# Kernel tuning notes

Hardware: AMD Instinct MI355X
Metric: run time of the kernel (lower is better)

Reference implementation:

```python
import jax, jax.numpy as jnp
import numpy as np

N = 50000        # nodes
E_RAND = 800000  # random edges; self-loops appended -> E = E_RAND + N
H = 4            # heads
D_IN = 256
D_HID = 64       # per-head hidden (H*D_HID == D_IN -> identity residual in layer 1)
D_OUT = 32       # classes per head
SLOPE = 0.2      # leaky-relu negative slope


def setup_inputs() -> dict:
    key = jax.random.key(0)
    ks = jax.random.split(key, 13)
    loops = jnp.arange(N, dtype=jnp.int32)
    src = jnp.concatenate([jax.random.randint(ks[0], (E_RAND,), 0, N, dtype=jnp.int32), loops])
    dst = jnp.concatenate([jax.random.randint(ks[1], (E_RAND,), 0, N, dtype=jnp.int32), loops])
    h = jax.random.normal(ks[2], (N, D_IN), dtype=jnp.float32)
    def w(k, shape, fan):
        return jax.random.normal(k, shape, dtype=jnp.float32) * (1.0 / np.sqrt(fan))
    return {
        "h": h, "src": src, "dst": dst,
        # layer 1 (tuple in_feats -> separate fc_src / fc_dst in dgl GATConv)
        "W1_src": w(ks[3], (D_IN, H * D_HID), D_IN),
        "W1_dst": w(ks[4], (D_IN, H * D_HID), D_IN),
        "al1": w(ks[5], (H, D_HID), D_HID),
        "ar1": w(ks[6], (H, D_HID), D_HID),
        # layer 2
        "W2_src": w(ks[7], (H * D_HID, H * D_OUT), H * D_HID),
        "W2_dst": w(ks[8], (H * D_HID, H * D_OUT), H * D_HID),
        "al2": w(ks[9], (H, D_OUT), D_OUT),
        "ar2": w(ks[10], (H, D_OUT), D_OUT),
        # residual projection for layer 2 (in_dim != heads*out)
        "Wres2": w(ks[11], (H * D_HID, H * D_OUT), H * D_HID),
    }


def gat_conv(h_node, src, dst, Ws, Wd, al, ar, heads, dout, resval):
    n = h_node.shape[0]
    fs = (h_node @ Ws).reshape(n, heads, dout)   # [N,H,D] projected src feats
    fd = (h_node @ Wd).reshape(n, heads, dout)
    el = jnp.sum(fs * al, axis=-1)               # [N,H]
    er = jnp.sum(fd * ar, axis=-1)               # [N,H]
    e = jax.nn.leaky_relu(el[src] + er[dst], SLOPE)           # [E,H] edge scores
    emax = jax.ops.segment_max(e, dst, num_segments=n)        # segment softmax over dst
    ex = jnp.exp(e - emax[dst])
    denom = jax.ops.segment_sum(ex, dst, num_segments=n)
    a = ex / denom[dst]                                        # [E,H] attention
    msg = fs[src] * a[:, :, None]                              # [E,H,D] gather * weight
    out = jax.ops.segment_sum(msg, dst, num_segments=n)       # [N,H,D] scatter-add
    return out + resval


def reference(h, src, dst, W1_src, W1_dst, al1, ar1, W2_src, W2_dst, al2, ar2, Wres2):
    # layer 1: identity residual (in_dim == heads*hidden), elu activation, flatten heads
    res1 = h.reshape(-1, H, D_HID)
    h1 = gat_conv(h, src, dst, W1_src, W1_dst, al1, ar1, H, D_HID, res1)
    h1 = jax.nn.elu(h1).reshape(-1, H * D_HID)
    # layer 2: linear residual, no activation, mean over heads
    res2 = (h1 @ Wres2).reshape(-1, H, D_OUT)
    h2 = gat_conv(h1, src, dst, W2_src, W2_dst, al2, ar2, H, D_OUT, res2)
    return h2.mean(axis=1)                                     # [N, num_classes]
```

## Files before the change

kernel.cpp:

```cpp
#include <hip/hip_runtime.h>
#include <hip/hip_bf16.h>

#define NN 50000
#define EE 850000
#define NBLK_SCAN 98

typedef unsigned short u16;
using short8 = __attribute__((ext_vector_type(8))) short;
using f32x4  = __attribute__((ext_vector_type(4))) float;

__device__ __forceinline__ float bf2f(u16 u) {
    union { unsigned int i; float f; } v; v.i = ((unsigned int)u) << 16; return v.f;
}
__device__ __forceinline__ u16 f2bf(float f) {
    __hip_bfloat16 h = __float2bfloat16(f);
    return *reinterpret_cast<u16*>(&h);
}

__device__ __forceinline__ float ld1(const void* X, size_t i, bool f32m) {
    return f32m ? ((const float*)X)[i] : bf2f(((const u16*)X)[i]);
}
__device__ __forceinline__ void load4(const void* X, size_t g, bool f32m, float o[4]) {
    if (f32m) {
        float4 v = ((const float4*)X)[g];
        o[0] = v.x; o[1] = v.y; o[2] = v.z; o[3] = v.w;
    } else {
        ushort4 v = ((const ushort4*)X)[g];
        o[0] = bf2f(v.x); o[1] = bf2f(v.y); o[2] = bf2f(v.z); o[3] = bf2f(v.w);
    }
}

__global__ void k_detect(const u16* __restrict__ hh, int* __restrict__ flag,
                         int* __restrict__ deg) {
    if (blockIdx.x != 0) {
        int i = (blockIdx.x - 1) * 256 + threadIdx.x;
        if (i < NN) deg[i] = 0;
        return;
    }
    __shared__ int sm[256];
    int t = threadIdx.x;
    int c = 0;
    for (int i = 0; i < 16; ++i) {
        u16 u = hh[t * 16 + i];
        int e = (u >> 7) & 0xFF;
        if (e != 0 && (e < 90 || e > 160)) ++c;
    }
    sm[t] = c;
    __syncthreads();
    for (int s = 128; s > 0; s >>= 1) {
        if (t < s) sm[t] += sm[t + s];
        __syncthreads();
    }
    if (t == 0) *flag = (sm[0] > 200) ? 1 : 0;
}

__global__ void k_prep(const void* __restrict__ W1s, const void* __restrict__ al1,
                       const void* __restrict__ W1d, const void* __restrict__ ar1,
                       const void* __restrict__ W2s, const void* __restrict__ al2,
                       const void* __restrict__ W2d, const void* __restrict__ ar2,
                       const void* __restrict__ Wres2, const int* __restrict__ dst,
                       u16* __restrict__ BT1, u16* __restrict__ BT2,
                       float* __restrict__ wl1, float* __restrict__ wr1,
                       float* __restrict__ wl2, float* __restrict__ wr2,
                       int* __restrict__ deg, const int* __restrict__ mode) {
    int bid = blockIdx.x;
    if (bid >= 528) {
        int e = (bid - 528) * 256 + threadIdx.x;
        if (e < EE) atomicAdd(&deg[dst[e]], 1);
        return;
    }
    bool f32m = (*mode) != 0;
    if (bid < 512) {
        int id = bid * 256 + threadIdx.x;
        int which = id >> 16;
        int rem = id & 65535;
        int n = rem >> 8, k = rem & 255;
        if (which == 0) {
            BT1[n * 256 + k] = f2bf(ld1(W1s, (size_t)k * 256 + n, f32m));
        } else {
            float v = (n < 128) ? ld1(W2s, (size_t)k * 128 + n, f32m)
                                : ld1(Wres2, (size_t)k * 128 + (n - 128), f32m);
            BT2[n * 256 + k] = f2bf(v);
        }
    } else {
        int id = (bid - 512) * 256 + threadIdx.x;
        int which = id >> 10;
        int rem = id & 1023;
        int k = rem >> 2, h = rem & 3;
        float s = 0.f;
        if (which == 0) {
            for (int d = 0; d < 64; ++d) s += ld1(W1s, k * 256 + h * 64 + d, f32m) * ld1(al1, h * 64 + d, f32m);
            wl1[k * 4 + h] = s;
        } else if (which == 1) {
            for (int d = 0; d < 64; ++d) s += ld1(W1d, k * 256 + h * 64 + d, f32m) * ld1(ar1, h * 64 + d, f32m);
            wr1[k * 4 + h] = s;
        } else if (which == 2) {
            for (int d = 0; d < 32; ++d) s += ld1(W2s, k * 128 + h * 32 + d, f32m) * ld1(al2, h * 32 + d, f32m);
            wl2[k * 4 + h] = s;
        } else {
            for (int d = 0; d < 32; ++d) s += ld1(W2d, k * 128 + h * 32 + d, f32m) * ld1(ar2, h * 32 + d, f32m);
            wr2[k * 4 + h] = s;
        }
    }
}

__global__ void k_scan1(const int* __restrict__ deg, int* __restrict__ rowptr,
                        int* __restrict__ bsum) {
    __shared__ int sm[512];
    int t = threadIdx.x;
    int i = blockIdx.x * 512 + t;
    int v = (i < NN) ? deg[i] : 0;
    int x = v;
    sm[t] = x;
    __syncthreads();
    for (int off = 1; off < 512; off <<= 1) {
        int y = (t >= off) ? sm[t - off] : 0;
        __syncthreads();
        x += y;
        sm[t] = x;
        __syncthreads();
    }
    if (i < NN) rowptr[i] = x - v;
    if (t == 511) bsum[blockIdx.x] = x;
}

__global__ void k_scan2(const int* __restrict__ bsum, int* __restrict__ boff) {
    __shared__ int sm[128];
    int t = threadIdx.x;
    int v = (t < NBLK_SCAN) ? bsum[t] : 0;
    int x = v;
    sm[t] = x;
    __syncthreads();
    for (int off = 1; off < 128; off <<= 1) {
        int y = (t >= off) ? sm[t - off] : 0;
        __syncthreads();
        x += y;
        sm[t] = x;
        __syncthreads();
    }
    if (t < NBLK_SCAN) boff[t] = x - v;
}

__global__ void k_scan3_eler1(int* __restrict__ rowptr, const int* __restrict__ boff,
                              int* __restrict__ cursor, const void* __restrict__ X,
                              const float* __restrict__ wl, const float* __restrict__ wr,
                              float* __restrict__ el, float* __restrict__ er,
                              const int* __restrict__ mode) {
    int bid = blockIdx.x;
    if (bid < 196) {
        int i = bid * 256 + threadIdx.x;
        if (i < NN) {
            int r = rowptr[i] + boff[i >> 9];
            rowptr[i] = r;
            cursor[i] = r;
            if (i == 0) rowptr[NN] = EE;
        }
        return;
    }
    bool f32m = (*mode) != 0;
    int wave = threadIdx.x >> 6, lane = threadIdx.x & 63;
    int node = (bid - 196) * 4 + wave;
    float a[4];
    load4(X, (size_t)node * 64 + lane, f32m, a);
    float accl[4] = {0, 0, 0, 0}, accr[4] = {0, 0, 0, 0};
    int k0 = lane * 4;
#pragma unroll
    for (int j = 0; j < 4; ++j) {
        float4 wlv = ((const float4*)wl)[k0 + j];
        float4 wrv = ((const float4*)wr)[k0 + j];
        accl[0] += a[j] * wlv.x; accl[1] += a[j] * wlv.y;
        accl[2] += a[j] * wlv.z; accl[3] += a[j] * wlv.w;
        accr[0] += a[j] * wrv.x; accr[1] += a[j] * wrv.y;
        accr[2] += a[j] * wrv.z; accr[3] += a[j] * wrv.w;
    }
#pragma unroll
    for (int off = 32; off > 0; off >>= 1) {
#pragma unroll
        for (int t = 0; t < 4; ++t) {
            accl[t] += __shfl_down(accl[t], off, 64);
            accr[t] += __shfl_down(accr[t], off, 64);
        }
    }
    if (lane == 0) {
        float4 vl = {accl[0], accl[1], accl[2], accl[3]};
        float4 vr = {accr[0], accr[1], accr[2], accr[3]};
        ((float4*)el)[node] = vl;
        ((float4*)er)[node] = vr;
    }
}

__global__ void k_scatter(const int* __restrict__ src, const int* __restrict__ dst,
                          int* __restrict__ cursor, int* __restrict__ csrc,
                          const float* __restrict__ el, const float* __restrict__ er,
                          u16* __restrict__ aw) {
    int e = blockIdx.x * 256 + threadIdx.x;
    if (e >= EE) return;
    int s = src[e], d = dst[e];
    int slot = atomicAdd(&cursor[d], 1);
    csrc[slot] = s;
    float4 eL = ((const float4*)el)[s];
    float4 eR = ((const float4*)er)[d];
    float ev[4] = {eL.x + eR.x, eL.y + eR.y, eL.z + eR.z, eL.w + eR.w};
    ushort4 o;
    u16* op = (u16*)&o;
#pragma unroll
    for (int t = 0; t < 4; ++t) {
        float x = ev[t];
        x = x > 0.f ? x : 0.2f * x;
        x = fminf(fmaxf(x, -60.f), 60.f);
        op[t] = f2bf(__expf(x));
    }
    ((ushort4*)aw)[slot] = o;
}

__global__ void k_gemm_mfma(const void* __restrict__ A, int aDual,
                            const u16* __restrict__ BT, u16* __restrict__ C,
                            const int* __restrict__ mode) {
    bool af32 = aDual && ((*mode) != 0);
    __shared__ u16 At[128 * 72];
    __shared__ u16 Bt[128 * 72];
    int t = threadIdx.x;
    int lane = t & 63, w = t >> 6;
    int mt = blockIdx.x >> 1, nt = blockIdx.x & 1;
    int m0 = mt * 128, n0 = nt * 128;
    int wr = (w >> 1) * 64, wc = (w & 1) * 64;
    f32x4 acc[4][4] = {};
    int q = lane >> 4, cl = lane & 15;

    for (int ph = 0; ph < 4; ++ph) {
        int kb = ph * 64;
        for (int it = 0; it < 4; ++it) {
            int c = it * 256 + t;
            int row = c >> 3, c8 = c & 7;
            int rowg = m0 + row;
            if (af32) {
                if (rowg < NN) {
                    const float* ap = (const float*)A + (size_t)rowg * 256 + kb + c8 * 8;
                    float4 v0 = ((const float4*)ap)[0];
                    float4 v1 = ((const float4*)ap)[1];
                    ushort4 lo = {f2bf(v0.x), f2bf(v0.y), f2bf(v0.z), f2bf(v0.w)};
                    ushort4 hi = {f2bf(v1.x), f2bf(v1.y), f2bf(v1.z), f2bf(v1.w)};
                    *(ushort4*)&At[row * 72 + c8 * 8] = lo;
                    *(ushort4*)&At[row * 72 + c8 * 8 + 4] = hi;
                } else {
                    ushort4 z = {0, 0, 0, 0};
                    *(ushort4*)&At[row * 72 + c8 * 8] = z;
                    *(ushort4*)&At[row * 72 + c8 * 8 + 4] = z;
                }
            } else {
                float4 av;
                if (rowg < NN) {
                    av = *(const float4*)((const u16*)A + (size_t)rowg * 256 + kb + c8 * 8);
                } else {
                    av = make_float4(0.f, 0.f, 0.f, 0.f);
                }
                *(float4*)&At[row * 72 + c8 * 8] = av;
            }
            float4 bv = *(const float4*)(BT + (size_t)(n0 + row) * 256 + kb + c8 * 8);
            *(float4*)&Bt[row * 72 + c8 * 8] = bv;
        }
        __syncthreads();
#pragma unroll
        for (int ks = 0; ks < 2; ++ks) {
            short8 af[4], bf[4];
#pragma unroll
            for (int i = 0; i < 4; ++i)
                af[i] = *(const short8*)&At[(wr + i * 16 + cl) * 72 + ks * 32 + q * 8];
#pragma unroll
            for (int j = 0; j < 4; ++j)
                bf[j] = *(const short8*)&Bt[(wc + j * 16 + cl) * 72 + ks * 32 + q * 8];
#pragma unroll
            for (int i = 0; i < 4; ++i)
#pragma unroll
                for (int j = 0; j < 4; ++j)
                    acc[i][j] = __builtin_amdgcn_mfma_f32_16x16x32_bf16(af[i], bf[j], acc[i][j], 0, 0, 0);
        }
        __syncthreads();
    }
#pragma unroll
    for (int i = 0; i < 4; ++i)
#pragma unroll
        for (int j = 0; j < 4; ++j)
#pragma unroll
            for (int r = 0; r < 4; ++r) {
                int mrow = m0 + wr + i * 16 + q * 4 + r;
                if (mrow < NN)
                    C[(size_t)mrow * 256 + n0 + wc + j * 16 + cl] = f2bf(acc[i][j][r]);
            }
}

__global__ void k_agg1(const int* __restrict__ rowptr, const int* __restrict__ csrc,
                       const u16* __restrict__ aw, const u16* __restrict__ fs,
                       const void* __restrict__ h_in, u16* __restrict__ h1,
                       const float* __restrict__ wl2, const float* __restrict__ wr2,
                       float* __restrict__ el2, float* __restrict__ er2,
                       const int* __restrict__ mode) {
    bool f32m = (*mode) != 0;
    int wave = threadIdx.x >> 6, lane = threadIdx.x & 63;
    int node = blockIdx.x * 4 + wave;
    int beg = rowptr[node], end = rowptr[node + 1];
    int head = lane >> 4;
    float a0 = 0.f, a1 = 0.f, a2 = 0.f, a3 = 0.f, ll = 0.f;
#pragma unroll 4
    for (int p = beg; p < end; ++p) {
        int s = csrc[p];
        float pw = bf2f(aw[(size_t)p * 4 + head]);
        ushort4 fv = *(const ushort4*)(fs + (size_t)s * 256 + lane * 4);
        ll += pw;
        a0 += pw * bf2f(fv.x);
        a1 += pw * bf2f(fv.y);
        a2 += pw * bf2f(fv.z);
        a3 += pw * bf2f(fv.w);
    }
    float rinv = 1.f / ll;
    float res[4];
    load4(h_in, (size_t)node * 64 + lane, f32m, res);
    float v0 = a0 * rinv + res[0], v1 = a1 * rinv + res[1];
    float v2 = a2 * rinv + res[2], v3 = a3 * rinv + res[3];
    v0 = v0 > 0.f ? v0 : __expf(v0) - 1.f;
    v1 = v1 > 0.f ? v1 : __expf(v1) - 1.f;
    v2 = v2 > 0.f ? v2 : __expf(v2) - 1.f;
    v3 = v3 > 0.f ? v3 : __expf(v3) - 1.f;
    ushort4 o = {f2bf(v0), f2bf(v1), f2bf(v2), f2bf(v3)};
    ((ushort4*)h1)[(size_t)node * 64 + lane] = o;
    float4 w0 = ((const float4*)wl2)[lane * 4 + 0];
    float4 w1 = ((const float4*)wl2)[lane * 4 + 1];
    float4 w2 = ((const float4*)wl2)[lane * 4 + 2];
    float4 w3 = ((const float4*)wl2)[lane * 4 + 3];
    float4 r0 = ((const float4*)wr2)[lane * 4 + 0];
    float4 r1 = ((const float4*)wr2)[lane * 4 + 1];
    float4 r2 = ((const float4*)wr2)[lane * 4 + 2];
    float4 r3 = ((const float4*)wr2)[lane * 4 + 3];
    float acl[4], acr[4];
    acl[0] = v0 * w0.x + v1 * w1.x + v2 * w2.x + v3 * w3.x;
    acl[1] = v0 * w0.y + v1 * w1.y + v2 * w2.y + v3 * w3.y;
    acl[2] = v0 * w0.z + v1 * w1.z + v2 * w2.z + v3 * w3.z;
    acl[3] = v0 * w0.w + v1 * w1.w + v2 * w2.w + v3 * w3.w;
    acr[0] = v0 * r0.x + v1 * r1.x + v2 * r2.x + v3 * r3.x;
    acr[1] = v0 * r0.y + v1 * r1.y + v2 * r2.y + v3 * r3.y;
    acr[2] = v0 * r0.z + v1 * r1.z + v2 * r2.z + v3 * r3.z;
    acr[3] = v0 * r0.w + v1 * r1.w + v2 * r2.w + v3 * r3.w;
#pragma unroll
    for (int off = 32; off > 0; off >>= 1) {
#pragma unroll
        for (int t = 0; t < 4; ++t) {
            acl[t] += __shfl_down(acl[t], off, 64);
            acr[t] += __shfl_down(acr[t], off, 64);
        }
    }
    if (lane == 0) {
        float4 vl = {acl[0], acl[1], acl[2], acl[3]};
        float4 vr = {acr[0], acr[1], acr[2], acr[3]};
        ((float4*)el2)[node] = vl;
        ((float4*)er2)[node] = vr;
    }
}

__global__ void k_agg2(const int* __restrict__ rowptr, const int* __restrict__ csrc,
                       const float* __restrict__ el, const float* __restrict__ er,
                       const u16* __restrict__ c2, void* __restrict__ out,
                       const int* __restrict__ mode) {
    bool f32m = (*mode) != 0;
    int wave = threadIdx.x >> 6, lane = threadIdx.x & 63;
    int node = blockIdx.x * 4 + wave;
    int beg = rowptr[node], end = rowptr[node + 1];
    int head = lane >> 4;
    float erh = er[node * 4 + head];
    float a0 = 0.f, a1 = 0.f, ll = 0.f;
#pragma unroll 2
    for (int p = beg; p < end; ++p) {
        int s = csrc[p];
        float e = el[s * 4 + head] + erh;
        e = e > 0.f ? e : 0.2f * e;
        e = fminf(fmaxf(e, -60.f), 60.f);
        float pw = __expf(e);
        ushort2 fv = *(const ushort2*)(c2 + (size_t)s * 256 + lane * 2);
        ll += pw;
        a0 += pw * bf2f(fv.x);
        a1 += pw * bf2f(fv.y);
    }
    float rinv = 1.f / ll;
    ushort2 rv = *(const ushort2*)(c2 + (size_t)node * 256 + 128 + lane * 2);
    float o0 = a0 * rinv + bf2f(rv.x);
    float o1 = a1 * rinv + bf2f(rv.y);
    o0 += __shfl_xor(o0, 16, 64); o0 += __shfl_xor(o0, 32, 64);
    o1 += __shfl_xor(o1, 16, 64); o1 += __shfl_xor(o1, 32, 64);
    if (lane < 16) {
        float v0 = 0.25f * o0, v1 = 0.25f * o1;
        size_t oi = (size_t)node * 32 + lane * 2;
        if (f32m) {
            ((float*)out)[oi] = v0;
            ((float*)out)[oi + 1] = v1;
        } else {
            ushort2 ov = {f2bf(v0), f2bf(v1)};
            *(ushort2*)((u16*)out + oi) = ov;
        }
    }
}

extern "C" void kernel_launch(void* const* d_in, const int* in_sizes, int n_in,
                              void* d_out, int out_size, void* d_ws, size_t ws_size,
                              hipStream_t stream) {
    int ih = 0, isrc = 1, idst = 2, iW1s = 3, iW1d = 4, ial1 = 5, iar1 = 6,
        iW2s = 7, iW2d = 8, ial2 = 9, iar2 = 10, iWres = 11;
    if (n_in >= 12 && in_sizes[0] != 12800000) {
        iW1d = 0; iW1s = 1; iW2d = 2; iW2s = 3; iWres = 4; ial1 = 5; ial2 = 6;
        iar1 = 7; iar2 = 8; idst = 9; ih = 10; isrc = 11;
    }
    const void* h     = d_in[ih];
    const int* src    = (const int*)d_in[isrc];
    const int* dst    = (const int*)d_in[idst];
    const void* W1s   = d_in[iW1s];
    const void* W1d   = d_in[iW1d];
    const void* al1   = d_in[ial1];
    const void* ar1   = d_in[iar1];
    const void* W2s   = d_in[iW2s];
    const void* W2d   = d_in[iW2d];
    const void* al2   = d_in[ial2];
    const void* ar2   = d_in[iar2];
    const void* Wres2 = d_in[iWres];

    char* w = (char*)d_ws;
    size_t off = 0;
    auto alloc = [&](size_t bytes) -> void* {
        void* p = w + off;
        off += (bytes + 255) & ~(size_t)255;
        return p;
    };
    int* mode   = (int*)alloc(256);
    float* wl1 = (float*)alloc(256 * 4 * 4);
    float* wr1 = (float*)alloc(256 * 4 * 4);
    float* wl2 = (float*)alloc(256 * 4 * 4);
    float* wr2 = (float*)alloc(256 * 4 * 4);
    int* deg    = (int*)alloc(NN * 4);
    int* cursor = (int*)alloc(NN * 4);
    int* rowptr = (int*)alloc((NN + 1) * 4);
    int* bsum   = (int*)alloc(NBLK_SCAN * 4);
    int* boff   = (int*)alloc(NBLK_SCAN * 4);
    int* csrc   = (int*)alloc((size_t)EE * 4);
    u16* aw     = (u16*)alloc((size_t)EE * 4 * 2);
    float* el1  = (float*)alloc((size_t)NN * 4 * 4);
    float* er1  = (float*)alloc((size_t)NN * 4 * 4);
    float* el2  = (float*)alloc((size_t)NN * 4 * 4);
    float* er2  = (float*)alloc((size_t)NN * 4 * 4);
    u16* BT1    = (u16*)alloc(256 * 256 * 2);
    u16* BT2    = (u16*)alloc(256 * 256 * 2);
    u16* fs1    = (u16*)alloc((size_t)NN * 256 * 2);
    u16* h1     = (u16*)alloc((size_t)NN * 256 * 2);
    u16* c2     = fs1;

    k_detect<<<197, 256, 0, stream>>>((const u16*)h, mode, deg);
    k_prep<<<528 + (EE + 255) / 256, 256, 0, stream>>>(
        W1s, al1, W1d, ar1, W2s, al2, W2d, ar2, Wres2, dst,
        BT1, BT2, wl1, wr1, wl2, wr2, deg, mode);
    k_scan1<<<NBLK_SCAN, 512, 0, stream>>>(deg, rowptr, bsum);
    k_scan2<<<1, 128, 0, stream>>>(bsum, boff);
    k_scan3_eler1<<<196 + NN / 4, 256, 0, stream>>>(rowptr, boff, cursor,
                                                    h, wl1, wr1, el1, er1, mode);
    k_scatter<<<(EE + 255) / 256, 256, 0, stream>>>(src, dst, cursor, csrc,
                                                    el1, er1, aw);
    k_gemm_mfma<<<782, 256, 0, stream>>>(h, 1, BT1, fs1, mode);
    k_agg1<<<NN / 4, 256, 0, stream>>>(rowptr, csrc, aw, fs1, h, h1,
                                       wl2, wr2, el2, er2, mode);
    k_gemm_mfma<<<782, 256, 0, stream>>>(h1, 0, BT2, c2, mode);
    k_agg2<<<NN / 4, 256, 0, stream>>>(rowptr, csrc, el2, er2, c2, d_out, mode);
}
```

Before: 403.1 us.

## Record edge rank during degree count; drop cursor atomics and precompute layer-2 weights

The degree-count atomic now returns each edge's rank within its destination, so CSR slots come from rowptr plus that rank and the second atomic pass through a cursor array goes away. The separate single-block scan kernel is folded into the rowptr fix-up, where each block sums the block totals from shared memory. Layer-2 attention exponentials are precomputed per edge by reusing the weight-generation kernel, so agg2 reads bf16 weights instead of gathering el and recomputing exp. Aggregation loop unroll factors go up. This costs an extra EE-sized eorder buffer plus an extra kernel launch, and layer-2 weights are now rounded to bf16.

```diff
diff --git a/kernel.cpp b/kernel.cpp
--- a/kernel.cpp
+++ b/kernel.cpp
@@ -62,11 +62,15 @@
                        u16* __restrict__ BT1, u16* __restrict__ BT2,
                        float* __restrict__ wl1, float* __restrict__ wr1,
                        float* __restrict__ wl2, float* __restrict__ wr2,
-                       int* __restrict__ deg, const int* __restrict__ mode) {
+                       int* __restrict__ deg, int* __restrict__ eorder,
+                       const int* __restrict__ mode) {
     int bid = blockIdx.x;
     if (bid >= 528) {
         int e = (bid - 528) * 256 + threadIdx.x;
-        if (e < EE) atomicAdd(&deg[dst[e]], 1);
+        if (e < EE) {
+            int r = atomicAdd(&deg[dst[e]], 1);
+            eorder[e] = r;
+        }
         return;
     }
     bool f32m = (*mode) != 0;
@@ -124,35 +128,23 @@
     if (t == 511) bsum[blockIdx.x] = x;
 }
 
-__global__ void k_scan2(const int* __restrict__ bsum, int* __restrict__ boff) {
-    __shared__ int sm[128];
-    int t = threadIdx.x;
-    int v = (t < NBLK_SCAN) ? bsum[t] : 0;
-    int x = v;
-    sm[t] = x;
-    __syncthreads();
-    for (int off = 1; off < 128; off <<= 1) {
-        int y = (t >= off) ? sm[t - off] : 0;
-        __syncthreads();
-        x += y;
-        sm[t] = x;
-        __syncthreads();
-    }
-    if (t < NBLK_SCAN) boff[t] = x - v;
-}
-
-__global__ void k_scan3_eler1(int* __restrict__ rowptr, const int* __restrict__ boff,
-                              int* __restrict__ cursor, const void* __restrict__ X,
+__global__ void k_scan3_eler1(int* __restrict__ rowptr, const int* __restrict__ bsum,
+                              const void* __restrict__ X,
                               const float* __restrict__ wl, const float* __restrict__ wr,
                               float* __restrict__ el, float* __restrict__ er,
                               const int* __restrict__ mode) {
     int bid = blockIdx.x;
     if (bid < 196) {
-        int i = bid * 256 + threadIdx.x;
+        __shared__ int sm[NBLK_SCAN];
+        int t = threadIdx.x;
+        if (t < NBLK_SCAN) sm[t] = bsum[t];
+        __syncthreads();
+        int g = bid >> 1;
+        int pre = 0;
+        for (int j = 0; j < g; ++j) pre += sm[j];
+        int i = bid * 256 + t;
         if (i < NN) {
-            int r = rowptr[i] + boff[i >> 9];
-            rowptr[i] = r;
-            cursor[i] = r;
+            rowptr[i] += pre;
             if (i == 0) rowptr[NN] = EE;
         }
         return;
@@ -189,15 +181,15 @@
     }
 }
 
-__global__ void k_scatter(const int* __restrict__ src, const int* __restrict__ dst,
-                          int* __restrict__ cursor, int* __restrict__ csrc,
-                          const float* __restrict__ el, const float* __restrict__ er,
-                          u16* __restrict__ aw) {
+__global__ void k_awgen(const int* __restrict__ src, const int* __restrict__ dst,
+                        const int* __restrict__ eorder, const int* __restrict__ rowptr,
+                        const float* __restrict__ el, const float* __restrict__ er,
+                        u16* __restrict__ aw, int* __restrict__ csrc, int writeCsrc) {
     int e = blockIdx.x * 256 + threadIdx.x;
     if (e >= EE) return;
     int s = src[e], d = dst[e];
-    int slot = atomicAdd(&cursor[d], 1);
-    csrc[slot] = s;
+    int slot = rowptr[d] + eorder[e];
+    if (writeCsrc) csrc[slot] = s;
     float4 eL = ((const float4*)el)[s];
     float4 eR = ((const float4*)er)[d];
     float ev[4] = {eL.x + eR.x, eL.y + eR.y, eL.z + eR.z, eL.w + eR.w};
@@ -301,7 +293,7 @@
     int beg = rowptr[node], end = rowptr[node + 1];
     int head = lane >> 4;
     float a0 = 0.f, a1 = 0.f, a2 = 0.f, a3 = 0.f, ll = 0.f;
-#pragma unroll 4
+#pragma unroll 8
     for (int p = beg; p < end; ++p) {
         int s = csrc[p];
         float pw = bf2f(aw[(size_t)p * 4 + head]);
@@ -357,23 +349,18 @@
 }
 
 __global__ void k_agg2(const int* __restrict__ rowptr, const int* __restrict__ csrc,
-                       const float* __restrict__ el, const float* __restrict__ er,
-                       const u16* __restrict__ c2, void* __restrict__ out,
-                       const int* __restrict__ mode) {
+                       const u16* __restrict__ aw, const u16* __restrict__ c2,
+                       void* __restrict__ out, const int* __restrict__ mode) {
     bool f32m = (*mode) != 0;
     int wave = threadIdx.x >> 6, lane = threadIdx.x & 63;
     int node = blockIdx.x * 4 + wave;
     int beg = rowptr[node], end = rowptr[node + 1];
     int head = lane >> 4;
-    float erh = er[node * 4 + head];
     float a0 = 0.f, a1 = 0.f, ll = 0.f;
-#pragma unroll 2
+#pragma unroll 8
     for (int p = beg; p < end; ++p) {
         int s = csrc[p];
-        float e = el[s * 4 + head] + erh;
-        e = e > 0.f ? e : 0.2f * e;
-        e = fminf(fmaxf(e, -60.f), 60.f);
-        float pw = __expf(e);
+        float pw = bf2f(aw[(size_t)p * 4 + head]);
         ushort2 fv = *(const ushort2*)(c2 + (size_t)s * 256 + lane * 2);
         ll += pw;
         a0 += pw * bf2f(fv.x);
@@ -433,10 +420,9 @@
     float* wl2 = (float*)alloc(256 * 4 * 4);
     float* wr2 = (float*)alloc(256 * 4 * 4);
     int* deg    = (int*)alloc(NN * 4);
-    int* cursor = (int*)alloc(NN * 4);
     int* rowptr = (int*)alloc((NN + 1) * 4);
     int* bsum   = (int*)alloc(NBLK_SCAN * 4);
-    int* boff   = (int*)alloc(NBLK_SCAN * 4);
+    int* eorder = (int*)alloc((size_t)EE * 4);
     int* csrc   = (int*)alloc((size_t)EE * 4);
     u16* aw     = (u16*)alloc((size_t)EE * 4 * 2);
     float* el1  = (float*)alloc((size_t)NN * 4 * 4);
@@ -452,16 +438,17 @@
     k_detect<<<197, 256, 0, stream>>>((const u16*)h, mode, deg);
     k_prep<<<528 + (EE + 255) / 256, 256, 0, stream>>>(
         W1s, al1, W1d, ar1, W2s, al2, W2d, ar2, Wres2, dst,
-        BT1, BT2, wl1, wr1, wl2, wr2, deg, mode);
+        BT1, BT2, wl1, wr1, wl2, wr2, deg, eorder, mode);
     k_scan1<<<NBLK_SCAN, 512, 0, stream>>>(deg, rowptr, bsum);
-    k_scan2<<<1, 128, 0, stream>>>(bsum, boff);
-    k_scan3_eler1<<<196 + NN / 4, 256, 0, stream>>>(rowptr, boff, cursor,
+    k_scan3_eler1<<<196 + NN / 4, 256, 0, stream>>>(rowptr, bsum,
                                                     h, wl1, wr1, el1, er1, mode);
-    k_scatter<<<(EE + 255) / 256, 256, 0, stream>>>(src, dst, cursor, csrc,
-                                                    el1, er1, aw);
+    k_awgen<<<(EE + 255) / 256, 256, 0, stream>>>(src, dst, eorder, rowptr,
+                                                  el1, er1, aw, csrc, 1);
     k_gemm_mfma<<<782, 256, 0, stream>>>(h, 1, BT1, fs1, mode);
     k_agg1<<<NN / 4, 256, 0, stream>>>(rowptr, csrc, aw, fs1, h, h1,
                                        wl2, wr2, el2, er2, mode);
     k_gemm_mfma<<<782, 256, 0, stream>>>(h1, 0, BT2, c2, mode);
-    k_agg2<<<NN / 4, 256, 0, stream>>>(rowptr, csrc, el2, er2, c2, d_out, mode);
-}
+    k_awgen<<<(EE + 255) / 256, 256, 0, stream>>>(src, dst, eorder, rowptr,
+                                                  el2, er2, aw, csrc, 0);
+    k_agg2<<<NN / 4, 256, 0, stream>>>(rowptr, csrc, aw, c2, d_out, mode);
+}
```

Measured after the change: 375.3 us. 6.9% less time.
